# Kernel optimization log

Measured on AMD Instinct MI355X. Metric: run time of the kernel, lower is better.

The kernel has to match this reference:

```python
import jax, jax.numpy as jnp
import numpy as np

COMMITMENT_BETA = 0.25


def setup_inputs() -> dict:
    key = jax.random.key(0)
    k1, k2 = jax.random.split(key)
    B, D, H, W = 32, 256, 32, 32
    NUM_CODES = 1024
    z = jax.random.normal(k1, (B, D, H, W), dtype=jnp.float32)
    codebook = jax.random.normal(k2, (NUM_CODES, D), dtype=jnp.float32)
    return {"z": z, "codebook": codebook}


def reference(z, codebook):
    # z: [B, D, H, W], codebook: [K, D]
    B, D, H, W = z.shape
    z_flat = jnp.transpose(z, (0, 2, 3, 1)).reshape(-1, D)  # [N, D]
    # squared euclidean distances: ||z||^2 - 2 z.W^T + ||W||^2  -> [N, K]
    d = (
        jnp.sum(z_flat * z_flat, axis=1, keepdims=True)
        - 2.0 * (z_flat @ codebook.T)
        + jnp.sum(codebook * codebook, axis=1)[None, :]
    )
    indices = jnp.argmin(d, axis=1)  # [N]
    z_q_flat = codebook[indices]  # [N, D] gather
    # commitment loss: mse(z_flat, stop_grad(z_q_flat))
    diff = z_flat - jax.lax.stop_gradient(z_q_flat)
    commitment_loss = jnp.mean(diff * diff)
    # straight-through estimator
    z_q_flat = z_flat + jax.lax.stop_gradient(z_q_flat - z_flat)
    z_q = jnp.transpose(z_q_flat.reshape(B, H, W, D), (0, 3, 1, 2))
    indices = indices.reshape(B, H, W)
    return z_q, indices, COMMITMENT_BETA * commitment_loss
```

## Files before the change

### kernel.cpp

```cpp
#include <hip/hip_runtime.h>
#include <hip/hip_bf16.h>
#include <hip/hip_fp16.h>

#define DD  256
#define HWD 1024
#define NN  32768
#define KK  1024
#define ZQ_SIZE (NN*DD)
#define IDX_OFF ZQ_SIZE
#define LOSS_OFF (ZQ_SIZE + NN)

#define CBH_OFF    0
#define CNORM_OFF  (KK*DD*2)
#define ZSQ_OFF    (CNORM_OFF + KK*4)
#define ROWREC_OFF (ZSQ_OFF + 2048)

#define DBIAS 512.0f
#define TH_REFINE 0.5f
#define LOSS_SCALE (0.25f / (float)ZQ_SIZE)

typedef __attribute__((ext_vector_type(8))) _Float16 h16x8;
typedef __attribute__((ext_vector_type(4))) float f32x4;

__device__ __forceinline__ void gload16(const void* g, void* l) {
    __builtin_amdgcn_global_load_lds(
        (const __attribute__((address_space(1))) void*)g,
        (__attribute__((address_space(3))) void*)l, 16, 0, 0);
}
__device__ __forceinline__ unsigned short f16u(float x) {
    _Float16 h = (_Float16)x;
    return *reinterpret_cast<unsigned short*>(&h);
}
__device__ __forceinline__ int swz(int row) {
    return (row & 15) ^ ((row >> 2) & 15);
}

__global__ __launch_bounds__(256)
void vq_prep_kernel(const float* __restrict__ cb, unsigned char* __restrict__ scratch) {
    _Float16* cbh = (_Float16*)(scratch + CBH_OFF);
    float* cn = (float*)(scratch + CNORM_OFF);
    int t = threadIdx.x;
    int row = blockIdx.x * 16 + (t >> 4);
    int dq  = t & 15;
    const float* rp = cb + (size_t)row * DD + dq * 16;
    float nrm = 0.f;
    __attribute__((aligned(16))) _Float16 h[16];
#pragma unroll
    for (int i = 0; i < 4; ++i) {
        float4 v = *(const float4*)(rp + i * 4);
        float xs[4] = {v.x, v.y, v.z, v.w};
#pragma unroll
        for (int j = 0; j < 4; ++j) {
            float x = xs[j];
            h[i * 4 + j] = (_Float16)x;
            nrm = fmaf(x, x, nrm);
        }
    }
    *(uint4*)&cbh[(size_t)row * DD + dq * 16]     = *(uint4*)&h[0];
    *(uint4*)&cbh[(size_t)row * DD + dq * 16 + 8] = *(uint4*)&h[8];
#pragma unroll
    for (int m = 1; m < 16; m <<= 1) nrm += __shfl_xor(nrm, m, 64);
    if (dq == 0) cn[row] = nrm + DBIAS;
}

__global__ __launch_bounds__(256) __attribute__((amdgpu_waves_per_eu(2, 2)))
void vq_mfma_argmin_kernel(const float* __restrict__ z, unsigned char* __restrict__ scratch) {
    const unsigned char* cbh_b = scratch + CBH_OFF;
    const float* cn_g = (const float*)(scratch + CNORM_OFF);
    float* zsqp = (float*)(scratch + ZSQ_OFF);
    float* rowrec = (float*)(scratch + ROWREC_OFF);

    __shared__ __attribute__((aligned(16))) short bufs[4 * 8192];
    __shared__ float cn_l[KK];
    __shared__ float zred[4];

    const int t    = threadIdx.x;
    const int w    = t >> 6;
    const int lane = t & 63;
    const int ln15 = lane & 15;
    const int lh   = lane >> 4;
    const int g     = w >> 1;
    const int khalf = w & 1;

    const int n0  = blockIdx.x * 64;
    const int b   = n0 >> 10;
    const int hw0 = n0 & 1023;

    const int ksub  = lane >> 5;
    const int chunk = lane & 31;

    const int klr   = khalf * 16 + ln15;
    const int rbase = klr * 256;
    const int rxor  = swz(klr) << 3;

    *(float4*)&cn_l[t * 4] = *(const float4*)(cn_g + t * 4);

    {
        short* zlds = bufs;
        const int zd = t >> 4;
        const int zq = t & 15;
        const float* zb = z + (size_t)b * DD * HWD + hw0 + zq * 4;
        float zsq = 0.f;
#pragma unroll
        for (int p = 0; p < 16; p += 2) {
            int d0 = zd * 16 + p;
            float4 va = *(const float4*)(zb + (size_t)(d0 + 0) * HWD);
            float4 vb = *(const float4*)(zb + (size_t)(d0 + 1) * HWD);
            zsq = fmaf(va.x, va.x, zsq); zsq = fmaf(va.y, va.y, zsq);
            zsq = fmaf(va.z, va.z, zsq); zsq = fmaf(va.w, va.w, zsq);
            zsq = fmaf(vb.x, vb.x, zsq); zsq = fmaf(vb.y, vb.y, zsq);
            zsq = fmaf(vb.z, vb.z, zsq); zsq = fmaf(vb.w, vb.w, zsq);
            float xa[4] = {va.x, va.y, va.z, va.w};
            float xb[4] = {vb.x, vb.y, vb.z, vb.w};
#pragma unroll
            for (int i = 0; i < 4; ++i) {
                int row = zq * 4 + i;
                int idx = row * 256 + (d0 ^ (swz(row) << 3));
                unsigned pk = (unsigned)f16u(xa[i]) | ((unsigned)f16u(xb[i]) << 16);
                *(unsigned*)&zlds[idx] = pk;
            }
        }
#pragma unroll
        for (int m = 1; m < 64; m <<= 1) zsq += __shfl_xor(zsq, m, 64);
        if (lane == 0) zred[w] = zsq;
    }
    __syncthreads();

    h16x8 ah[2][8];
#pragma unroll
    for (int nf = 0; nf < 2; ++nf) {
#pragma unroll
        for (int ds = 0; ds < 8; ++ds) {
            int row = g * 32 + nf * 16 + ln15;
            int d0  = ds * 32 + lh * 8;
            ah[nf][ds] = *(const h16x8*)&bufs[row * 256 + (d0 ^ (swz(row) << 3))];
        }
    }
    if (t == 0) zsqp[blockIdx.x] = (zred[0] + zred[1]) + (zred[2] + zred[3]);
    __syncthreads();

    auto STAGE = [&](int tt) {
#pragma unroll
        for (int si = 0; si < 4; ++si) {
            int s  = w * 4 + si;
            int kl = s * 2 + ksub;
            const unsigned char* src = cbh_b
                + (size_t)(tt * 32 + kl) * 512 + ((chunk ^ swz(kl)) << 4);
            gload16(src, &bufs[(tt & 3) * 8192 + s * 512]);
        }
    };

    float v1[8], v2[8];
#pragma unroll
    for (int s = 0; s < 8; ++s) { v1[s] = 3e38f; v2[s] = 3e38f; }

    auto COMPUTE = [&](int kt) {
        const short* cbt = &bufs[(kt & 3) * 8192];
        const float cnv = cn_l[kt * 32 + klr];
        const unsigned kbits = (unsigned)(kt * 32 + klr);
        f32x4 c0 = {0.f,0.f,0.f,0.f}, c1 = c0, c2 = c0, c3 = c0;
#pragma unroll
        for (int ds = 0; ds < 8; ds += 2) {
            const int ib0 = rbase + (((ds + 0) * 32 + lh * 8) ^ rxor);
            const int ib1 = rbase + (((ds + 1) * 32 + lh * 8) ^ rxor);
            h16x8 b0 = *(const h16x8*)&cbt[ib0];
            h16x8 b1 = *(const h16x8*)&cbt[ib1];
            c0 = __builtin_amdgcn_mfma_f32_16x16x32_f16(ah[0][ds + 0], b0, c0, 0, 0, 0);
            c2 = __builtin_amdgcn_mfma_f32_16x16x32_f16(ah[1][ds + 0], b0, c2, 0, 0, 0);
            c1 = __builtin_amdgcn_mfma_f32_16x16x32_f16(ah[0][ds + 1], b1, c1, 0, 0, 0);
            c3 = __builtin_amdgcn_mfma_f32_16x16x32_f16(ah[1][ds + 1], b1, c3, 0, 0, 0);
        }
        f32x4 s0 = c0 + c1, s1 = c2 + c3;
#pragma unroll
        for (int s = 0; s < 8; ++s) {
            float a = (s < 4) ? s0[s] : s1[s - 4];
            float dist = fmaf(-2.f, a, cnv);
            float pd = __uint_as_float((__float_as_uint(dist) & 0xFFFFFC00u) | kbits);
            v2[s] = fminf(fmaxf(pd, v1[s]), v2[s]);
            v1[s] = fminf(pd, v1[s]);
        }
    };

    STAGE(0); STAGE(1); STAGE(2);

    for (int kt = 0; kt < 29; ++kt) {
        asm volatile("s_waitcnt vmcnt(8)" ::: "memory");
        __builtin_amdgcn_sched_barrier(0);
        __builtin_amdgcn_s_barrier();
        __builtin_amdgcn_sched_barrier(0);
        STAGE(kt + 3);
        COMPUTE(kt);
    }
    asm volatile("s_waitcnt vmcnt(8)" ::: "memory");
    __builtin_amdgcn_sched_barrier(0);
    __builtin_amdgcn_s_barrier();
    __builtin_amdgcn_sched_barrier(0);
    COMPUTE(29);
    asm volatile("s_waitcnt vmcnt(4)" ::: "memory");
    __builtin_amdgcn_sched_barrier(0);
    __builtin_amdgcn_s_barrier();
    __builtin_amdgcn_sched_barrier(0);
    COMPUTE(30);
    asm volatile("s_waitcnt vmcnt(0)" ::: "memory");
    __builtin_amdgcn_sched_barrier(0);
    __builtin_amdgcn_s_barrier();
    __builtin_amdgcn_sched_barrier(0);
    COMPUTE(31);

    __syncthreads();
    float* redv = (float*)bufs;
#pragma unroll
    for (int s = 0; s < 8; ++s) {
        int nf = s >> 2, r = s & 3;
        int rowb = g * 32 + nf * 16 + lh * 4 + r;
        redv[klr * 65 + rowb]        = v1[s];
        redv[(32 + klr) * 65 + rowb] = v2[s];
    }
    __syncthreads();

    const int p = t >> 6, row = t & 63;
    float w1 = 3e38f, w2 = 3e38f, w3 = 3e38f;
#pragma unroll
    for (int q = 0; q < 16; ++q) {
        float v = redv[(p * 16 + q) * 65 + row];
        w3 = fminf(fmaxf(v, w2), w3);
        w2 = fminf(fmaxf(v, w1), w2);
        w1 = fminf(v, w1);
    }
    __syncthreads();
    {
        float* pv = (float*)bufs;
        int base = (p * 64 + row) * 3;
        pv[base + 0] = w1; pv[base + 1] = w2; pv[base + 2] = w3;
    }
    __syncthreads();
    if (t < 64) {
        const float* pv = (const float*)bufs;
        float u1 = 3e38f, u2 = 3e38f, u3 = 3e38f;
#pragma unroll
        for (int i = 0; i < 12; ++i) {
            float v = pv[((i / 3) * 64 + t) * 3 + (i % 3)];
            u3 = fminf(fmaxf(v, u2), u3);
            u2 = fminf(fmaxf(v, u1), u2);
            u1 = fminf(v, u1);
        }
        float4 rec; rec.x = u1; rec.y = u2; rec.z = u3; rec.w = 0.f;
        *(float4*)&rowrec[(size_t)(n0 + t) * 4] = rec;
    }
}

__global__ __launch_bounds__(256)
void vq_refine_kernel(const float* __restrict__ z, const float* __restrict__ cb,
                      const unsigned char* __restrict__ scratch, float* __restrict__ idx_out,
                      float* __restrict__ lossp) {
    const float* rowrec = (const float*)(scratch + ROWREC_OFF);
    const float* cn_g = (const float*)(scratch + CNORM_OFF);
    const float* zsqp = (const float*)(scratch + ZSQ_OFF);
    int n = blockIdx.x * 256 + threadIdx.x;
    int lane = threadIdx.x & 63;

    float4 rr = *(const float4*)&rowrec[(size_t)n * 4];
    unsigned b1 = __float_as_uint(rr.x);
    bool flag = (rr.y - rr.x) <= TH_REFINE;
    float lp = 0.f;
    if (!flag) {
        idx_out[n] = (float)(b1 & 1023u);
        lp = __uint_as_float(b1 & 0xFFFFFC00u) - DBIAS;
    }

    unsigned long long mask = __ballot(flag);
    while (mask) {
        int li = __ffsll(mask) - 1;
        mask &= mask - 1;
        int nn  = __shfl(n, li);
        int kk1 = (int)(__float_as_uint(__shfl(rr.x, li)) & 1023u);
        int kk2 = (int)(__float_as_uint(__shfl(rr.y, li)) & 1023u);
        int kk3 = (int)(__float_as_uint(__shfl(rr.z, li)) & 1023u);
        int bb = nn >> 10, hw = nn & 1023;
        const float* zp  = z  + (size_t)bb * DD * HWD + hw;
        const float* c1p = cb + (size_t)kk1 * DD;
        const float* c2p = cb + (size_t)kk2 * DD;
        const float* c3p = cb + (size_t)kk3 * DD;
        float s1 = 0.f, s2 = 0.f, s3 = 0.f;
#pragma unroll
        for (int j = 0; j < 4; ++j) {
            int d = lane + 64 * j;
            float zv = zp[(size_t)d * HWD];
            s1 = fmaf(zv, c1p[d], s1);
            s2 = fmaf(zv, c2p[d], s2);
            s3 = fmaf(zv, c3p[d], s3);
        }
#pragma unroll
        for (int m = 32; m >= 1; m >>= 1) {
            s1 += __shfl_xor(s1, m, 64);
            s2 += __shfl_xor(s2, m, 64);
            s3 += __shfl_xor(s3, m, 64);
        }
        float e1 = (cn_g[kk1] - DBIAS) - 2.f * s1;
        float e2 = (cn_g[kk2] - DBIAS) - 2.f * s2;
        float e3 = (cn_g[kk3] - DBIAS) - 2.f * s3;
        float dch = e1; int kch = kk1;
        if (e2 < dch || (e2 == dch && kk2 < kch)) { dch = e2; kch = kk2; }
        if (e3 < dch || (e3 == dch && kk3 < kch)) { dch = e3; kch = kk3; }
        if (lane == 0) { idx_out[nn] = (float)kch; lp += dch; }
    }

    if (blockIdx.x == 0) {
        const float2 zv = *(const float2*)&zsqp[threadIdx.x * 2];
        lp += zv.x + zv.y;
    }
#pragma unroll
    for (int m = 32; m >= 1; m >>= 1) lp += __shfl_xor(lp, m, 64);
    __shared__ float bl[4];
    if (lane == 0) bl[threadIdx.x >> 6] = lp;
    __syncthreads();
    if (threadIdx.x == 0)
        atomicAdd(lossp, (bl[0] + bl[1] + bl[2] + bl[3]) * LOSS_SCALE);
}

__global__ __launch_bounds__(256)
void vq_gather_kernel(const float* __restrict__ cb, float* __restrict__ out) {
    const float* idxf = out + IDX_OFF;
    __shared__ float crow[64][257];
    __shared__ int kidx[64];
    int t = threadIdx.x;
    int w = t >> 6, lane = t & 63;
    int n0 = blockIdx.x * 64;
    int b = n0 >> 10, hw0 = n0 & 1023;
    if (t < 64) kidx[t] = (int)idxf[n0 + t];
    __syncthreads();
    for (int i = 0; i < 16; ++i) {
        int r = w * 16 + i;
        int k = kidx[r];
        float4 v = *(const float4*)(cb + (size_t)k * DD + lane * 4);
        crow[r][lane * 4 + 0] = v.x; crow[r][lane * 4 + 1] = v.y;
        crow[r][lane * 4 + 2] = v.z; crow[r][lane * 4 + 3] = v.w;
    }
    __syncthreads();
    const int zph = t >> 6, hwl = t & 63;
#pragma unroll 4
    for (int dd = 0; dd < 64; ++dd) {
        int d = dd * 4 + zph;
        size_t o = (size_t)b * (DD * HWD) + (size_t)d * HWD + hw0 + hwl;
        out[o] = crow[hwl][d];
    }
}

extern "C" void kernel_launch(void* const* d_in, const int* in_sizes, int n_in,
                              void* d_out, int out_size, void* d_ws, size_t ws_size,
                              hipStream_t stream) {
    const float* z  = (const float*)d_in[0];
    const float* cb = (const float*)d_in[1];
    float* out = (float*)d_out;
    unsigned char* scratch = (unsigned char*)d_out;

    hipMemsetAsync((void*)(out + LOSS_OFF), 0, sizeof(float), stream);

    vq_prep_kernel<<<64, 256, 0, stream>>>(cb, scratch);
    vq_mfma_argmin_kernel<<<512, 256, 0, stream>>>(z, scratch);
    vq_refine_kernel<<<128, 256, 0, stream>>>(z, cb, scratch, out + IDX_OFF, out + LOSS_OFF);
    vq_gather_kernel<<<512, 256, 0, stream>>>(cb, out);
}
```

Measured before the change: 67.93 us.

## Split codebook search across two blocks per row tile and merge in refine

The argmin kernel now launches twice as many blocks, with each block scanning half of the codebook (512 codes) for a 64-row tile. Partial top-3 records go to separate rowrec slices, and the refine kernel merges the two into a global top-3. The LDS pipeline drops from 4 to 3 stages and waves_per_eu rises to 3 so more blocks fit per CU. The cost is loading and converting z twice, the extra merge work, and a shallower prefetch depth. The rowrec region now holds two slices, which must fit in the scratch space.

```diff
diff --git a/kernel.cpp b/kernel.cpp
--- a/kernel.cpp
+++ b/kernel.cpp
@@ -63,15 +63,15 @@
     if (dq == 0) cn[row] = nrm + DBIAS;
 }
 
-__global__ __launch_bounds__(256) __attribute__((amdgpu_waves_per_eu(2, 2)))
+__global__ __launch_bounds__(256) __attribute__((amdgpu_waves_per_eu(3, 3)))
 void vq_mfma_argmin_kernel(const float* __restrict__ z, unsigned char* __restrict__ scratch) {
     const unsigned char* cbh_b = scratch + CBH_OFF;
     const float* cn_g = (const float*)(scratch + CNORM_OFF);
     float* zsqp = (float*)(scratch + ZSQ_OFF);
     float* rowrec = (float*)(scratch + ROWREC_OFF);
 
-    __shared__ __attribute__((aligned(16))) short bufs[4 * 8192];
-    __shared__ float cn_l[KK];
+    __shared__ __attribute__((aligned(16))) short bufs[3 * 8192];
+    __shared__ float cn_l[512];
     __shared__ float zred[4];
 
     const int t    = threadIdx.x;
@@ -82,7 +82,9 @@
     const int g     = w >> 1;
     const int khalf = w & 1;
 
-    const int n0  = blockIdx.x * 64;
+    const int kq  = blockIdx.x & 1;
+    const int rt  = blockIdx.x >> 1;
+    const int n0  = rt * 64;
     const int b   = n0 >> 10;
     const int hw0 = n0 & 1023;
 
@@ -93,7 +95,7 @@
     const int rbase = klr * 256;
     const int rxor  = swz(klr) << 3;
 
-    *(float4*)&cn_l[t * 4] = *(const float4*)(cn_g + t * 4);
+    *(float2*)&cn_l[t * 2] = *(const float2*)(cn_g + kq * 512 + t * 2);
 
     {
         short* zlds = bufs;
@@ -136,7 +138,7 @@
             ah[nf][ds] = *(const h16x8*)&bufs[row * 256 + (d0 ^ (swz(row) << 3))];
         }
     }
-    if (t == 0) zsqp[blockIdx.x] = (zred[0] + zred[1]) + (zred[2] + zred[3]);
+    if (kq == 0 && t == 0) zsqp[rt] = (zred[0] + zred[1]) + (zred[2] + zred[3]);
     __syncthreads();
 
     auto STAGE = [&](int tt) {
@@ -145,8 +147,8 @@
             int s  = w * 4 + si;
             int kl = s * 2 + ksub;
             const unsigned char* src = cbh_b
-                + (size_t)(tt * 32 + kl) * 512 + ((chunk ^ swz(kl)) << 4);
-            gload16(src, &bufs[(tt & 3) * 8192 + s * 512]);
+                + (size_t)(kq * 512 + tt * 32 + kl) * 512 + ((chunk ^ swz(kl)) << 4);
+            gload16(src, &bufs[(tt % 3) * 8192 + s * 512]);
         }
     };
 
@@ -155,9 +157,9 @@
     for (int s = 0; s < 8; ++s) { v1[s] = 3e38f; v2[s] = 3e38f; }
 
     auto COMPUTE = [&](int kt) {
-        const short* cbt = &bufs[(kt & 3) * 8192];
+        const short* cbt = &bufs[(kt % 3) * 8192];
         const float cnv = cn_l[kt * 32 + klr];
-        const unsigned kbits = (unsigned)(kt * 32 + klr);
+        const unsigned kbits = (unsigned)(kq * 512 + kt * 32 + klr);
         f32x4 c0 = {0.f,0.f,0.f,0.f}, c1 = c0, c2 = c0, c3 = c0;
 #pragma unroll
         for (int ds = 0; ds < 8; ds += 2) {
@@ -181,31 +183,26 @@
         }
     };
 
-    STAGE(0); STAGE(1); STAGE(2);
-
-    for (int kt = 0; kt < 29; ++kt) {
-        asm volatile("s_waitcnt vmcnt(8)" ::: "memory");
+    STAGE(0); STAGE(1);
+
+    for (int kt = 0; kt < 14; ++kt) {
+        asm volatile("s_waitcnt vmcnt(4)" ::: "memory");
         __builtin_amdgcn_sched_barrier(0);
         __builtin_amdgcn_s_barrier();
         __builtin_amdgcn_sched_barrier(0);
-        STAGE(kt + 3);
+        STAGE(kt + 2);
         COMPUTE(kt);
     }
-    asm volatile("s_waitcnt vmcnt(8)" ::: "memory");
-    __builtin_amdgcn_sched_barrier(0);
-    __builtin_amdgcn_s_barrier();
-    __builtin_amdgcn_sched_barrier(0);
-    COMPUTE(29);
     asm volatile("s_waitcnt vmcnt(4)" ::: "memory");
     __builtin_amdgcn_sched_barrier(0);
     __builtin_amdgcn_s_barrier();
     __builtin_amdgcn_sched_barrier(0);
-    COMPUTE(30);
+    COMPUTE(14);
     asm volatile("s_waitcnt vmcnt(0)" ::: "memory");
     __builtin_amdgcn_sched_barrier(0);
     __builtin_amdgcn_s_barrier();
     __builtin_amdgcn_sched_barrier(0);
-    COMPUTE(31);
+    COMPUTE(15);
 
     __syncthreads();
     float* redv = (float*)bufs;
@@ -245,7 +242,7 @@
             u1 = fminf(v, u1);
         }
         float4 rec; rec.x = u1; rec.y = u2; rec.z = u3; rec.w = 0.f;
-        *(float4*)&rowrec[(size_t)(n0 + t) * 4] = rec;
+        *(float4*)&rowrec[((size_t)kq * NN + n0 + t) * 4] = rec;
     }
 }
 
@@ -259,11 +256,22 @@
     int n = blockIdx.x * 256 + threadIdx.x;
     int lane = threadIdx.x & 63;
 
-    float4 rr = *(const float4*)&rowrec[(size_t)n * 4];
-    unsigned b1 = __float_as_uint(rr.x);
-    bool flag = (rr.y - rr.x) <= TH_REFINE;
+    float4 r0 = *(const float4*)&rowrec[((size_t)0 * NN + n) * 4];
+    float4 r1 = *(const float4*)&rowrec[((size_t)1 * NN + n) * 4];
+    float u1 = 3e38f, u2 = 3e38f, u3 = 3e38f;
+    float cand[6] = {r0.x, r0.y, r0.z, r1.x, r1.y, r1.z};
+#pragma unroll
+    for (int i = 0; i < 6; ++i) {
+        float v = cand[i];
+        u3 = fminf(fmaxf(v, u2), u3);
+        u2 = fminf(fmaxf(v, u1), u2);
+        u1 = fminf(v, u1);
+    }
+
+    bool flag = (u2 - u1) <= TH_REFINE;
     float lp = 0.f;
     if (!flag) {
+        unsigned b1 = __float_as_uint(u1);
         idx_out[n] = (float)(b1 & 1023u);
         lp = __uint_as_float(b1 & 0xFFFFFC00u) - DBIAS;
     }
@@ -273,9 +281,9 @@
         int li = __ffsll(mask) - 1;
         mask &= mask - 1;
         int nn  = __shfl(n, li);
-        int kk1 = (int)(__float_as_uint(__shfl(rr.x, li)) & 1023u);
-        int kk2 = (int)(__float_as_uint(__shfl(rr.y, li)) & 1023u);
-        int kk3 = (int)(__float_as_uint(__shfl(rr.z, li)) & 1023u);
+        int kk1 = (int)(__float_as_uint(__shfl(u1, li)) & 1023u);
+        int kk2 = (int)(__float_as_uint(__shfl(u2, li)) & 1023u);
+        int kk3 = (int)(__float_as_uint(__shfl(u3, li)) & 1023u);
         int bb = nn >> 10, hw = nn & 1023;
         const float* zp  = z  + (size_t)bb * DD * HWD + hw;
         const float* c1p = cb + (size_t)kk1 * DD;
@@ -357,7 +365,7 @@
     hipMemsetAsync((void*)(out + LOSS_OFF), 0, sizeof(float), stream);
 
     vq_prep_kernel<<<64, 256, 0, stream>>>(cb, scratch);
-    vq_mfma_argmin_kernel<<<512, 256, 0, stream>>>(z, scratch);
+    vq_mfma_argmin_kernel<<<1024, 256, 0, stream>>>(z, scratch);
     vq_refine_kernel<<<128, 256, 0, stream>>>(z, cb, scratch, out + IDX_OFF, out + LOSS_OFF);
     vq_gather_kernel<<<512, 256, 0, stream>>>(cb, out);
 }
```

Result: slower. 70.47 us (+3.7%).
